# Optimization experiments

Measured on AMD Instinct MI355X. Metric: run time of the kernel, lower is better.

## Reference

```python
import jax, jax.numpy as jnp
import numpy as np

BS, NC, CN, DN = 8, 1024, 64, 64
GH, GW = 32, 32
ALPHA, BPC = 4, 4
G = 8
IN_LO, IN_HI = 0, ALPHA
OUT_LO, OUT_HI = ALPHA, 2 * ALPHA
B_LO, B_HI = 2 * ALPHA, 2 * ALPHA + BPC
HS, HM, HMOD = 256, 256, 128
MOD_IN = 3 * DN + 2 + BPC
MOD_OUT = DN + BPC


def setup_inputs():
    key = jax.random.key(0)
    ks = iter(jax.random.split(key, 40))
    def nrm(shape, s=0.05):
        return jax.random.normal(next(ks), shape, dtype=jnp.float32) * s
    return {
        "x": nrm((BS, NC * DN), 1.0),
        "h": nrm((BS, NC, CN, DN), 0.01),
        "msg": nrm((BS, NC, CN, DN), 0.1),
        "W": nrm((BS, NC, CN, CN), 0.1),
        "decay_logit": jnp.zeros((BS, NC, CN), jnp.float32),
        "cell_context": jnp.zeros((BS, NC, DN), jnp.float32),
        "border_gate_logit": jnp.zeros((BS, NC, BPC), jnp.float32),
        "neuron_id": nrm((NC, CN, DN), 0.02),
        "state_w1": nrm((HS, 2 * DN)), "state_b1": jnp.zeros((HS,), jnp.float32),
        "state_gs1": jnp.ones((G, HS), jnp.float32), "state_gb1": jnp.zeros((G, HS), jnp.float32),
        "state_w2": nrm((DN, HS)), "state_b2": jnp.zeros((DN,), jnp.float32),
        "state_gs2": jnp.ones((G, DN), jnp.float32), "state_gb2": jnp.zeros((G, DN), jnp.float32),
        "msg_w1": nrm((HM, DN)), "msg_b1": jnp.zeros((HM,), jnp.float32),
        "msg_gs1": jnp.ones((G, HM), jnp.float32), "msg_gb1": jnp.zeros((G, HM), jnp.float32),
        "msg_w2": nrm((DN, HM)), "msg_b2": jnp.zeros((DN,), jnp.float32),
        "msg_gs2": jnp.ones((G, DN), jnp.float32), "msg_gb2": jnp.zeros((G, DN), jnp.float32),
        "inject_w": nrm((G, ALPHA * DN, DN)), "inject_b": jnp.zeros((G, ALPHA * DN), jnp.float32),
        "mod_w1": nrm((NC, MOD_IN, HMOD)), "mod_b1": jnp.zeros((NC, HMOD), jnp.float32),
        "mod_w2": nrm((NC, HMOD, MOD_OUT), 0.01), "mod_b2": jnp.zeros((NC, MOD_OUT), jnp.float32),
        "cell_to_group": jnp.arange(NC, dtype=jnp.int32) % G,
    }


def _grouped_mlp(x, c2g, w1, b1, gs1, gb1, w2, b2, gs2, gb2):
    # x: [B, NC, CN, F]; group-specific affine modulation after each linear.
    hid = jnp.einsum('bcnf,hf->bcnh', x, w1) + b1
    hid = jnp.tanh(hid * gs1[c2g][None, :, None, :] + gb1[c2g][None, :, None, :])
    out = jnp.einsum('bcnh,dh->bcnd', hid, w2) + b2
    return jnp.tanh(out * gs2[c2g][None, :, None, :] + gb2[c2g][None, :, None, :])


def reference(x, h, msg, W, decay_logit, cell_context, border_gate_logit, neuron_id,
              state_w1, state_b1, state_gs1, state_gb1, state_w2, state_b2, state_gs2, state_gb2,
              msg_w1, msg_b1, msg_gs1, msg_gb1, msg_w2, msg_b2, msg_gs2, msg_gb2,
              inject_w, inject_b, mod_w1, mod_b1, mod_w2, mod_b2, cell_to_group):
    c2g = cell_to_group
    # 1) dense message passing inside each cell: received = W @ msg
    received = jnp.einsum('bcnm,bcmd->bcnd', W, msg)
    # 2) inject external input into input ports (per-group orthogonal-init projections)
    cell_slice = x.reshape(BS, NC, DN)
    iw, ib = inject_w[c2g], inject_b[c2g]                      # [NC, alpha*DN, DN], [NC, alpha*DN]
    inject = jnp.einsum('bni,noi->bno', cell_slice, iw) + ib   # [BS, NC, alpha*DN]
    received = received.at[:, :, IN_LO:IN_HI].add(inject.reshape(BS, NC, ALPHA, DN))
    # 3) fixed geometric border exchange between neighboring grid cells
    border = msg[:, :, B_LO:B_HI].reshape(BS, GH, GW, BPC, DN)
    incoming = jnp.zeros_like(border)
    incoming = incoming.at[:, 1:, :, 0].set(border[:, :-1, :, 1])
    incoming = incoming.at[:, :-1, :, 1].set(border[:, 1:, :, 0])
    incoming = incoming.at[:, :, 1:, 2].set(border[:, :, :-1, 3])
    incoming = incoming.at[:, :, :-1, 3].set(border[:, :, 1:, 2])
    incoming = incoming.reshape(BS, NC, BPC, DN)
    border_gate = jax.nn.sigmoid(border_gate_logit)[..., None]
    received = received.at[:, :, B_LO:B_HI].add(border_gate * incoming)
    # 4) gated recurrent state update
    decay = jax.nn.sigmoid(decay_logit)[..., None]
    cand = _grouped_mlp(jnp.concatenate([received, h], axis=-1), c2g,
                        state_w1, state_b1, state_gs1, state_gb1,
                        state_w2, state_b2, state_gs2, state_gb2)
    h_new = decay * h + (1.0 - decay) * cand
    # 5) emit new messages (+ per-neuron identity embedding)
    msg_new = _grouped_mlp(h_new, c2g, msg_w1, msg_b1, msg_gs1, msg_gb1,
                           msg_w2, msg_b2, msg_gs2, msg_gb2) + neuron_id[None]
    # 6) readout from output ports
    readout = (msg_new[:, :, OUT_LO:OUT_HI].sum(axis=2) * (ALPHA ** -0.5)).reshape(BS, -1)
    # 7) per-cell modulation MLP (distinct weights per cell)
    h_mean = h_new.mean(axis=2)
    msg_mean = msg_new.mean(axis=2)
    W_row = jnp.abs(W).mean(axis=-1).mean(axis=2, keepdims=True)
    decay_mean = decay_logit.mean(axis=2, keepdims=True)
    feats = jnp.concatenate([h_mean, msg_mean, W_row, decay_mean,
                             cell_context, border_gate_logit], axis=-1)   # [BS, NC, MOD_IN]
    hid = jnp.tanh(jnp.einsum('bcf,cfh->bch', feats, mod_w1) + mod_b1)
    mod = jnp.einsum('bch,cho->bco', hid, mod_w2) + mod_b2                 # [BS, NC, MOD_OUT]
    cell_context_new = cell_context + mod[..., :DN]
    border_gate_logit_new = border_gate_logit + mod[..., DN:]
    return readout, h_new, msg_new, cell_context_new, border_gate_logit_new
```

## Files before the change

kernel.cpp:

```cpp
#include <hip/hip_runtime.h>

#define NCC 1024
#define MODIN 198
#define MODOUT 68
#define HMODL 128

typedef __attribute__((ext_vector_type(8))) short s8v;
typedef __attribute__((ext_vector_type(4))) float f4v;
typedef unsigned short ushort_t;
typedef unsigned int uint_t;

#define OFF_SW1 0
#define OFF_SW2 32768
#define OFF_MW1 49152
#define OFF_MW2 65536
#define FEATS_BYTE_OFF 262144

__device__ __forceinline__ float fast_tanh(float x) {
    const float e = __builtin_amdgcn_exp2f(x * 2.885390081777927f);
    const float r = __builtin_amdgcn_rcpf(e + 1.f);
    return fmaf(-2.f, r, 1.f);
}
__device__ __forceinline__ float fast_sigmoid(float x) {
    const float e = __builtin_amdgcn_exp2f(x * -1.4426950408889634f);
    return __builtin_amdgcn_rcpf(e + 1.f);
}
__device__ __forceinline__ ushort_t f2bf(float x) {
    uint_t u = __builtin_bit_cast(uint_t, x);
    u += 0x7FFFu + ((u >> 16) & 1u);
    return (ushort_t)(u >> 16);
}
__device__ __forceinline__ uint_t pk2(float a, float b) {
    return (uint_t)f2bf(a) | ((uint_t)f2bf(b) << 16);
}
#define SWZ(byteoff, row) ((byteoff) ^ (((row) & 7) << 4))

__global__ __launch_bounds__(256)
void mg_cvtw(const float* __restrict__ sw1, const float* __restrict__ sw2,
             const float* __restrict__ mw1, const float* __restrict__ mw2,
             ushort_t* __restrict__ o) {
    const int i = blockIdx.x * 256 + threadIdx.x;
    float v;
    if (i < 32768)      v = sw1[i];
    else if (i < 49152) v = sw2[i - 32768];
    else if (i < 65536) v = mw1[i - 49152];
    else                v = mw2[i - 65536];
    o[i] = f2bf(v);
}

__global__ __launch_bounds__(256, 4)
void mg_inject(const float* __restrict__ xp, const float* __restrict__ iw,
               const float* __restrict__ ibias, const int* __restrict__ c2g,
               float* __restrict__ injb) {
    const int c = blockIdx.x, t = threadIdx.x;
    const int g = c2g[c];
    __shared__ float s_x[8][64];
    for (int idx = t; idx < 512; idx += 256)
        s_x[idx >> 6][idx & 63] = xp[(size_t)(idx >> 6) * (NCC * 64) + c * 64 + (idx & 63)];
    __syncthreads();
    const float* wrow = iw + (size_t)g * 16384 + t * 64;
    float a0 = 0.f, a1 = 0.f, a2 = 0.f, a3 = 0.f, a4 = 0.f, a5 = 0.f, a6 = 0.f, a7 = 0.f;
    #pragma unroll
    for (int i = 0; i < 64; i += 4) {
        const float4 w4 = *(const float4*)(wrow + i);
        const float4 x0 = *(const float4*)&s_x[0][i];
        const float4 x1 = *(const float4*)&s_x[1][i];
        const float4 x2 = *(const float4*)&s_x[2][i];
        const float4 x3 = *(const float4*)&s_x[3][i];
        const float4 x4 = *(const float4*)&s_x[4][i];
        const float4 x5 = *(const float4*)&s_x[5][i];
        const float4 x6 = *(const float4*)&s_x[6][i];
        const float4 x7 = *(const float4*)&s_x[7][i];
        a0 = fmaf(w4.x, x0.x, a0); a0 = fmaf(w4.y, x0.y, a0); a0 = fmaf(w4.z, x0.z, a0); a0 = fmaf(w4.w, x0.w, a0);
        a1 = fmaf(w4.x, x1.x, a1); a1 = fmaf(w4.y, x1.y, a1); a1 = fmaf(w4.z, x1.z, a1); a1 = fmaf(w4.w, x1.w, a1);
        a2 = fmaf(w4.x, x2.x, a2); a2 = fmaf(w4.y, x2.y, a2); a2 = fmaf(w4.z, x2.z, a2); a2 = fmaf(w4.w, x2.w, a2);
        a3 = fmaf(w4.x, x3.x, a3); a3 = fmaf(w4.y, x3.y, a3); a3 = fmaf(w4.z, x3.z, a3); a3 = fmaf(w4.w, x3.w, a3);
        a4 = fmaf(w4.x, x4.x, a4); a4 = fmaf(w4.y, x4.y, a4); a4 = fmaf(w4.z, x4.z, a4); a4 = fmaf(w4.w, x4.w, a4);
        a5 = fmaf(w4.x, x5.x, a5); a5 = fmaf(w4.y, x5.y, a5); a5 = fmaf(w4.z, x5.z, a5); a5 = fmaf(w4.w, x5.w, a5);
        a6 = fmaf(w4.x, x6.x, a6); a6 = fmaf(w4.y, x6.y, a6); a6 = fmaf(w4.z, x6.z, a6); a6 = fmaf(w4.w, x6.w, a6);
        a7 = fmaf(w4.x, x7.x, a7); a7 = fmaf(w4.y, x7.y, a7); a7 = fmaf(w4.z, x7.z, a7); a7 = fmaf(w4.w, x7.w, a7);
    }
    const float bv = ibias[g * 256 + t];
    const float acc[8] = {a0, a1, a2, a3, a4, a5, a6, a7};
    #pragma unroll
    for (int b = 0; b < 8; b++)
        injb[((size_t)b * NCC + c) * 4096 + t] = acc[b] + bv;
}

__global__ __launch_bounds__(512, 4)
void mg_cell_kernel(
    const float* __restrict__ hp,   const float* __restrict__ msgp,
    const float* __restrict__ Wp,   const float* __restrict__ decayp,
    const float* __restrict__ bglp, const float* __restrict__ nidp,
    const float* __restrict__ sb1,  const float* __restrict__ sgs1,
    const float* __restrict__ sgb1, const float* __restrict__ sb2,
    const float* __restrict__ sgs2, const float* __restrict__ sgb2,
    const float* __restrict__ mb1,  const float* __restrict__ mgs1,
    const float* __restrict__ mgb1, const float* __restrict__ mb2,
    const float* __restrict__ mgs2, const float* __restrict__ mgb2,
    const int*   __restrict__ c2g,  const ushort_t* __restrict__ wb,
    float* __restrict__ out_read, float* __restrict__ out_h,
    float* __restrict__ out_msg,  float* __restrict__ wsf)
{
    const int t  = threadIdx.x;
    const int bc = blockIdx.x;
    const int b  = bc >> 10, c = bc & 1023;
    const int gh = c >> 5, gwc = c & 31;
    const int lane = t & 63, w = t >> 6;
    const int cl = lane & 15, q = lane >> 4;
    const int g  = c2g[c];
    const size_t tile = (size_t)bc * 4096;

    __shared__ ushort_t sHid[8192];
    __shared__ ushort_t sIn[8192];
    __shared__ float s_scr[256];
    __shared__ float s_dec[64];
    __shared__ float s_wsum[8];
    __shared__ float s_dsum;

    ushort_t* sW    = sHid;
    ushort_t* sMsgT = sHid + 4096;

    {
        const int n = t >> 3, m0 = (t & 7) * 8;
        const float* src = Wp + tile + n * 64 + m0;
        const float4 v0 = *(const float4*)(src);
        const float4 v1 = *(const float4*)(src + 4);
        float wsum = fabsf(v0.x) + fabsf(v0.y) + fabsf(v0.z) + fabsf(v0.w)
                   + fabsf(v1.x) + fabsf(v1.y) + fabsf(v1.z) + fabsf(v1.w);
        *(uint_t*)((char*)sW + SWZ(n * 128 + (m0 + 0) * 2, n)) = pk2(v0.x, v0.y);
        *(uint_t*)((char*)sW + SWZ(n * 128 + (m0 + 2) * 2, n)) = pk2(v0.z, v0.w);
        *(uint_t*)((char*)sW + SWZ(n * 128 + (m0 + 4) * 2, n)) = pk2(v1.x, v1.y);
        *(uint_t*)((char*)sW + SWZ(n * 128 + (m0 + 6) * 2, n)) = pk2(v1.z, v1.w);
        #pragma unroll
        for (int off = 32; off > 0; off >>= 1) wsum += __shfl_down(wsum, off);
        if (lane == 0) s_wsum[w] = wsum;
    }
    #pragma unroll
    for (int i = 0; i < 2; i++) {
        const int m = (t >> 4) + i * 32, d0 = (t & 15) * 4;
        const float4 v = *(const float4*)(msgp + tile + (size_t)m * 64 + d0);
        *(ushort_t*)((char*)sMsgT + SWZ((d0 + 0) * 128 + m * 2, d0 + 0)) = f2bf(v.x);
        *(ushort_t*)((char*)sMsgT + SWZ((d0 + 1) * 128 + m * 2, d0 + 1)) = f2bf(v.y);
        *(ushort_t*)((char*)sMsgT + SWZ((d0 + 2) * 128 + m * 2, d0 + 2)) = f2bf(v.z);
        *(ushort_t*)((char*)sMsgT + SWZ((d0 + 3) * 128 + m * 2, d0 + 3)) = f2bf(v.w);
    }
    #pragma unroll
    for (int i = 0; i < 2; i++) {
        const int n = (t >> 4) + i * 32, d0 = (t & 15) * 4;
        const float4 v = *(const float4*)(hp + tile + (size_t)n * 64 + d0);
        *(uint_t*)((char*)sIn + SWZ(n * 256 + (64 + d0) * 2, n))     = pk2(v.x, v.y);
        *(uint_t*)((char*)sIn + SWZ(n * 256 + (64 + d0 + 2) * 2, n)) = pk2(v.z, v.w);
    }
    if (t < 256) {
        const int p = w, dd = lane;
        int ok, nc2, qq;
        if      (p == 0) { ok = (gh > 0);   nc2 = c - 32; qq = 1; }
        else if (p == 1) { ok = (gh < 31);  nc2 = c + 32; qq = 0; }
        else if (p == 2) { ok = (gwc > 0);  nc2 = c - 1;  qq = 3; }
        else             { ok = (gwc < 31); nc2 = c + 1;  qq = 2; }
        float v = 0.f;
        if (ok) v = msgp[((size_t)b * NCC + nc2) * 4096 + (8 + qq) * 64 + dd];
        s_scr[p * 64 + dd] = fast_sigmoid(bglp[(size_t)bc * 4 + p]) * v;
    }
    if (w == 4) {
        const float dl = decayp[(size_t)bc * 64 + lane];
        s_dec[lane] = fast_sigmoid(dl);
        float v = dl;
        #pragma unroll
        for (int off = 32; off > 0; off >>= 1) v += __shfl_down(v, off);
        if (lane == 0) s_dsum = v;
    }
    __syncthreads();

    const f4v fzero = {0.f, 0.f, 0.f, 0.f};
    const int d  = 16 * (w & 3) + cl;
    const int rh = w >> 2;

    {
        f4v wm[2] = {fzero, fzero};
        float injv[4] = {0.f, 0.f, 0.f, 0.f};
        if (rh == 0 && q == 0) {
            #pragma unroll
            for (int r = 0; r < 4; r++) injv[r] = out_h[tile + r * 64 + d];
        }
        __builtin_amdgcn_s_setprio(1);
        #pragma unroll
        for (int ks = 0; ks < 2; ks++) {
            const int k0 = ks * 32 + q * 8;
            const s8v bf = *(const s8v*)((const char*)sMsgT + SWZ(d * 128 + k0 * 2, d));
            #pragma unroll
            for (int rt2 = 0; rt2 < 2; rt2++) {
                const int ar = (rh * 2 + rt2) * 16 + cl;
                const s8v af = *(const s8v*)((const char*)sW + SWZ(ar * 128 + k0 * 2, ar));
                wm[rt2] = __builtin_amdgcn_mfma_f32_16x16x32_bf16(af, bf, wm[rt2], 0, 0, 0);
            }
        }
        __builtin_amdgcn_s_setprio(0);
        #pragma unroll
        for (int rt2 = 0; rt2 < 2; rt2++)
            #pragma unroll
            for (int r = 0; r < 4; r++) {
                const int n = (rh * 2 + rt2) * 16 + q * 4 + r;
                float v = wm[rt2][r];
                if (n < 4)                 v += injv[r];
                else if (n >= 8 && n < 12) v += s_scr[(n - 8) * 64 + d];
                *(ushort_t*)((char*)sIn + SWZ(n * 256 + d * 2, n)) = f2bf(v);
            }
    }
    __syncthreads();

    {
        f4v a2[2][2];
        a2[0][0] = fzero; a2[0][1] = fzero; a2[1][0] = fzero; a2[1][1] = fzero;
        const ushort_t* wb1 = wb + OFF_SW1;
        const ushort_t* wb2 = wb + OFF_SW2;
        #pragma unroll
        for (int p = 0; p < 2; p++) {
            {
                f4v acc[4] = {fzero, fzero, fzero, fzero};
                const int lc = 16 * w + cl;
                const int hcol = p * 128 + lc;
                __builtin_amdgcn_s_setprio(1);
                #pragma unroll
                for (int ks = 0; ks < 4; ks++) {
                    const int k0 = ks * 32 + q * 8;
                    const s8v bf = *(const s8v*)(wb1 + (size_t)hcol * 128 + k0);
                    #pragma unroll
                    for (int rt = 0; rt < 4; rt++) {
                        const int ar = rt * 16 + cl;
                        const s8v af = *(const s8v*)((const char*)sIn + SWZ(ar * 256 + k0 * 2, ar));
                        acc[rt] = __builtin_amdgcn_mfma_f32_16x16x32_bf16(af, bf, acc[rt], 0, 0, 0);
                    }
                }
                __builtin_amdgcn_s_setprio(0);
                const float b1 = sb1[hcol], g1 = sgs1[g * 256 + hcol], o1 = sgb1[g * 256 + hcol];
                #pragma unroll
                for (int rt = 0; rt < 4; rt++)
                    #pragma unroll
                    for (int r = 0; r < 4; r++) {
                        const int n = rt * 16 + q * 4 + r;
                        const float vv = fast_tanh(fmaf(acc[rt][r] + b1, g1, o1));
                        *(ushort_t*)((char*)sHid + SWZ(n * 256 + lc * 2, n)) = f2bf(vv);
                    }
            }
            __syncthreads();
            {
                __builtin_amdgcn_s_setprio(1);
                #pragma unroll
                for (int ks = 0; ks < 4; ks++) {
                    const int k0 = ks * 32 + q * 8;
                    const s8v bf = *(const s8v*)(wb2 + (size_t)d * 256 + p * 128 + k0);
                    #pragma unroll
                    for (int rt2 = 0; rt2 < 2; rt2++) {
                        const int ar = (rh * 2 + rt2) * 16 + cl;
                        const s8v af = *(const s8v*)((const char*)sHid + SWZ(ar * 256 + k0 * 2, ar));
                        a2[rt2][ks & 1] = __builtin_amdgcn_mfma_f32_16x16x32_bf16(af, bf, a2[rt2][ks & 1], 0, 0, 0);
                    }
                }
                __builtin_amdgcn_s_setprio(0);
            }
            if (p == 0) __syncthreads();
        }
        const float b2 = sb2[d], g2 = sgs2[g * 64 + d], o2 = sgb2[g * 64 + d];
        float hsum = 0.f;
        #pragma unroll
        for (int rt2 = 0; rt2 < 2; rt2++)
            #pragma unroll
            for (int r = 0; r < 4; r++) {
                const int n = (rh * 2 + rt2) * 16 + q * 4 + r;
                const float cand = fast_tanh(fmaf(a2[rt2][0][r] + a2[rt2][1][r] + b2, g2, o2));
                const ushort_t hu = *(const ushort_t*)((const char*)sIn + SWZ(n * 256 + (64 + d) * 2, n));
                const float hv = __builtin_bit_cast(float, (uint_t)hu << 16);
                const float hn = fmaf(s_dec[n], hv - cand, cand);
                out_h[tile + (size_t)n * 64 + d] = hn;
                *(ushort_t*)((char*)sIn + SWZ(n * 256 + d * 2, n)) = f2bf(hn);
                hsum += hn;
            }
        hsum += __shfl_xor(hsum, 16);
        hsum += __shfl_xor(hsum, 32);
        if (q == 0) s_scr[rh * 64 + d] = hsum;
    }
    __syncthreads();

    {
        float nv[8];
        #pragma unroll
        for (int rt2 = 0; rt2 < 2; rt2++)
            #pragma unroll
            for (int r = 0; r < 4; r++) {
                const int n = (rh * 2 + rt2) * 16 + q * 4 + r;
                nv[rt2 * 4 + r] = nidp[(size_t)c * 4096 + (size_t)n * 64 + d];
            }
        f4v a6[2][2];
        a6[0][0] = fzero; a6[0][1] = fzero; a6[1][0] = fzero; a6[1][1] = fzero;
        const ushort_t* wm1 = wb + OFF_MW1;
        const ushort_t* wm2 = wb + OFF_MW2;
        #pragma unroll
        for (int p = 0; p < 2; p++) {
            {
                f4v acc[4] = {fzero, fzero, fzero, fzero};
                const int lc = 16 * w + cl;
                const int hcol = p * 128 + lc;
                __builtin_amdgcn_s_setprio(1);
                #pragma unroll
                for (int ks = 0; ks < 2; ks++) {
                    const int k0 = ks * 32 + q * 8;
                    const s8v bf = *(const s8v*)(wm1 + (size_t)hcol * 64 + k0);
                    #pragma unroll
                    for (int rt = 0; rt < 4; rt++) {
                        const int ar = rt * 16 + cl;
                        const s8v af = *(const s8v*)((const char*)sIn + SWZ(ar * 256 + k0 * 2, ar));
                        acc[rt] = __builtin_amdgcn_mfma_f32_16x16x32_bf16(af, bf, acc[rt], 0, 0, 0);
                    }
                }
                __builtin_amdgcn_s_setprio(0);
                const float b1 = mb1[hcol], g1 = mgs1[g * 256 + hcol], o1 = mgb1[g * 256 + hcol];
                #pragma unroll
                for (int rt = 0; rt < 4; rt++)
                    #pragma unroll
                    for (int r = 0; r < 4; r++) {
                        const int n = rt * 16 + q * 4 + r;
                        const float vv = fast_tanh(fmaf(acc[rt][r] + b1, g1, o1));
                        *(ushort_t*)((char*)sHid + SWZ(n * 256 + lc * 2, n)) = f2bf(vv);
                    }
            }
            __syncthreads();
            {
                __builtin_amdgcn_s_setprio(1);
                #pragma unroll
                for (int ks = 0; ks < 4; ks++) {
                    const int k0 = ks * 32 + q * 8;
                    const s8v bf = *(const s8v*)(wm2 + (size_t)d * 256 + p * 128 + k0);
                    #pragma unroll
                    for (int rt2 = 0; rt2 < 2; rt2++) {
                        const int ar = (rh * 2 + rt2) * 16 + cl;
                        const s8v af = *(const s8v*)((const char*)sHid + SWZ(ar * 256 + k0 * 2, ar));
                        a6[rt2][ks & 1] = __builtin_amdgcn_mfma_f32_16x16x32_bf16(af, bf, a6[rt2][ks & 1], 0, 0, 0);
                    }
                }
                __builtin_amdgcn_s_setprio(0);
            }
            if (p == 0) __syncthreads();
        }
        const float b2 = mb2[d], g2 = mgs2[g * 64 + d], o2 = mgb2[g * 64 + d];
        float msum = 0.f, ro = 0.f;
        #pragma unroll
        for (int rt2 = 0; rt2 < 2; rt2++)
            #pragma unroll
            for (int r = 0; r < 4; r++) {
                const int n = (rh * 2 + rt2) * 16 + q * 4 + r;
                const float mv = fast_tanh(fmaf(a6[rt2][0][r] + a6[rt2][1][r] + b2, g2, o2))
                                 + nv[rt2 * 4 + r];
                out_msg[tile + (size_t)n * 64 + d] = mv;
                msum += mv;
                if (rt2 == 0 && q == 1 && rh == 0) ro += mv;
            }
        msum += __shfl_xor(msum, 16);
        msum += __shfl_xor(msum, 32);
        if (q == 0) s_scr[128 + rh * 64 + d] = msum;
        if (rh == 0 && q == 1) out_read[((size_t)b * NCC + c) * 64 + d] = ro * 0.5f;
    }
    __syncthreads();

    if (t < 132) {
        float v = 0.f;
        if (t < 64)        v = (s_scr[t] + s_scr[64 + t]) * (1.f / 64.f);
        else if (t < 128)  v = (s_scr[64 + t] + s_scr[128 + t]) * (1.f / 64.f);
        else if (t == 128) v = (s_wsum[0] + s_wsum[1] + s_wsum[2] + s_wsum[3]
                              + s_wsum[4] + s_wsum[5] + s_wsum[6] + s_wsum[7]) * (1.f / 4096.f);
        else if (t == 129) v = s_dsum * (1.f / 64.f);
        wsf[(size_t)bc * 132 + t] = v;
    }
}

__global__ __launch_bounds__(256, 2)
void mg_mod_kernel(
    const float* __restrict__ wsf,   const float* __restrict__ modw1,
    const float* __restrict__ modb1, const float* __restrict__ modw2,
    const float* __restrict__ modb2, const float* __restrict__ ctxp,
    const float* __restrict__ bglp,  float* __restrict__ out_ctx,
    float* __restrict__ out_bg)
{
    const int c = blockIdx.x;
    const int t = threadIdx.x;
    __shared__ float s_f[8][MODIN];
    __shared__ float s_h2[8][HMODL];

    for (int k = t; k < 8 * MODIN; k += 256) {
        const int b = k / MODIN, f = k - b * MODIN;
        float v;
        if (f < 130)      v = wsf[((size_t)b * NCC + c) * 132 + f];
        else if (f < 194) v = ctxp[((size_t)b * NCC + c) * 64 + (f - 130)];
        else              v = bglp[((size_t)b * NCC + c) * 4 + (f - 194)];
        s_f[b][f] = v;
    }
    __syncthreads();

    {
        const int hh = t & 127, bh = (t >> 7) * 4;
        float a0 = 0.f, a1 = 0.f, a2 = 0.f, a3 = 0.f;
        const float* wp = modw1 + (size_t)c * MODIN * HMODL + hh;
        for (int f = 0; f < MODIN; f++) {
            const float wv = wp[(size_t)f * HMODL];
            a0 = fmaf(s_f[bh + 0][f], wv, a0);
            a1 = fmaf(s_f[bh + 1][f], wv, a1);
            a2 = fmaf(s_f[bh + 2][f], wv, a2);
            a3 = fmaf(s_f[bh + 3][f], wv, a3);
        }
        const float bv = modb1[(size_t)c * HMODL + hh];
        s_h2[bh + 0][hh] = fast_tanh(a0 + bv);
        s_h2[bh + 1][hh] = fast_tanh(a1 + bv);
        s_h2[bh + 2][hh] = fast_tanh(a2 + bv);
        s_h2[bh + 3][hh] = fast_tanh(a3 + bv);
    }
    __syncthreads();

    for (int idx = t; idx < 8 * MODOUT; idx += 256) {
        const int b = idx / MODOUT, o = idx - b * MODOUT;
        float acc = modb2[(size_t)c * MODOUT + o];
        const float* wp = modw2 + (size_t)c * HMODL * MODOUT + o;
        const float* hrow = s_h2[b];
        for (int hh = 0; hh < HMODL; hh++)
            acc = fmaf(hrow[hh], wp[(size_t)hh * MODOUT], acc);
        if (o < 64)
            out_ctx[((size_t)b * NCC + c) * 64 + o] =
                ctxp[((size_t)b * NCC + c) * 64 + o] + acc;
        else
            out_bg[((size_t)b * NCC + c) * 4 + (o - 64)] =
                bglp[((size_t)b * NCC + c) * 4 + (o - 64)] + acc;
    }
}

extern "C" void kernel_launch(void* const* d_in, const int* in_sizes, int n_in,
                              void* d_out, int out_size, void* d_ws, size_t ws_size,
                              hipStream_t stream) {
    const float* xp     = (const float*)d_in[0];
    const float* hp     = (const float*)d_in[1];
    const float* msgp   = (const float*)d_in[2];
    const float* Wp     = (const float*)d_in[3];
    const float* decayp = (const float*)d_in[4];
    const float* ctxp   = (const float*)d_in[5];
    const float* bglp   = (const float*)d_in[6];
    const float* nidp   = (const float*)d_in[7];
    const float* sw1    = (const float*)d_in[8];
    const float* sb1    = (const float*)d_in[9];
    const float* sgs1   = (const float*)d_in[10];
    const float* sgb1   = (const float*)d_in[11];
    const float* sw2    = (const float*)d_in[12];
    const float* sb2    = (const float*)d_in[13];
    const float* sgs2   = (const float*)d_in[14];
    const float* sgb2   = (const float*)d_in[15];
    const float* mw1    = (const float*)d_in[16];
    const float* mb1    = (const float*)d_in[17];
    const float* mgs1   = (const float*)d_in[18];
    const float* mgb1   = (const float*)d_in[19];
    const float* mw2    = (const float*)d_in[20];
    const float* mb2    = (const float*)d_in[21];
    const float* mgs2   = (const float*)d_in[22];
    const float* mgb2   = (const float*)d_in[23];
    const float* iw     = (const float*)d_in[24];
    const float* ibias  = (const float*)d_in[25];
    const float* modw1  = (const float*)d_in[26];
    const float* modb1  = (const float*)d_in[27];
    const float* modw2  = (const float*)d_in[28];
    const float* modb2  = (const float*)d_in[29];
    const int*   c2g    = (const int*)d_in[30];

    float* out      = (float*)d_out;
    float* out_read = out;
    float* out_h    = out_read + 524288;
    float* out_msg  = out_h + 33554432;
    float* out_ctx  = out_msg + 33554432;
    float* out_bg   = out_ctx + 524288;

    ushort_t* wb  = (ushort_t*)d_ws;
    float*    wsf = (float*)((char*)d_ws + FEATS_BYTE_OFF);

    mg_cvtw<<<320, 256, 0, stream>>>(sw1, sw2, mw1, mw2, wb);

    mg_inject<<<1024, 256, 0, stream>>>(xp, iw, ibias, c2g, out_h);

    mg_cell_kernel<<<8192, 512, 0, stream>>>(
        hp, msgp, Wp, decayp, bglp, nidp,
        sb1, sgs1, sgb1, sb2, sgs2, sgb2,
        mb1, mgs1, mgb1, mb2, mgs2, mgb2,
        c2g, wb, out_read, out_h, out_msg, wsf);

    mg_mod_kernel<<<1024, 256, 0, stream>>>(
        wsf, modw1, modb1, modw2, modb2, ctxp, bglp, out_ctx, out_bg);
}
```

Measured before the change: 465.5 us.

## Swap MFMA operand roles so accumulators hold contiguous features for vectorized stores

Transposes every MFMA in the step kernel by swapping the A and B operands, so each lane's four accumulator values span four consecutive feature columns instead of four neuron rows. This lets the epilogues use float4 global loads and stores for h, msg, neuron_id and readout, packed 64-bit bf16 LDS writes, and float4 bias/scale loads. It replaces scattered scalar stores and 2-byte LDS writes with wider accesses. In exchange, the row reductions need a 4-step 16-lane shuffle tree per component instead of two shuffles, plus extra shuffles for the readout sum.

```diff
diff --git a/kernel.cpp b/kernel.cpp
--- a/kernel.cpp
+++ b/kernel.cpp
@@ -174,39 +174,39 @@
     __syncthreads();
 
     const f4v fzero = {0.f, 0.f, 0.f, 0.f};
-    const int d  = 16 * (w & 3) + cl;
+    const int d0 = 16 * (w & 3) + q * 4;
+    const int dA = 16 * (w & 3) + cl;
     const int rh = w >> 2;
 
     {
         f4v wm[2] = {fzero, fzero};
-        float injv[4] = {0.f, 0.f, 0.f, 0.f};
-        if (rh == 0 && q == 0) {
-            #pragma unroll
-            for (int r = 0; r < 4; r++) injv[r] = out_h[tile + r * 64 + d];
-        }
         __builtin_amdgcn_s_setprio(1);
         #pragma unroll
         for (int ks = 0; ks < 2; ks++) {
             const int k0 = ks * 32 + q * 8;
-            const s8v bf = *(const s8v*)((const char*)sMsgT + SWZ(d * 128 + k0 * 2, d));
+            const s8v am = *(const s8v*)((const char*)sMsgT + SWZ(dA * 128 + k0 * 2, dA));
             #pragma unroll
-            for (int rt2 = 0; rt2 < 2; rt2++) {
-                const int ar = (rh * 2 + rt2) * 16 + cl;
-                const s8v af = *(const s8v*)((const char*)sW + SWZ(ar * 128 + k0 * 2, ar));
-                wm[rt2] = __builtin_amdgcn_mfma_f32_16x16x32_bf16(af, bf, wm[rt2], 0, 0, 0);
+            for (int nt = 0; nt < 2; nt++) {
+                const int ar = (rh * 2 + nt) * 16 + cl;
+                const s8v bw = *(const s8v*)((const char*)sW + SWZ(ar * 128 + k0 * 2, ar));
+                wm[nt] = __builtin_amdgcn_mfma_f32_16x16x32_bf16(am, bw, wm[nt], 0, 0, 0);
             }
         }
         __builtin_amdgcn_s_setprio(0);
         #pragma unroll
-        for (int rt2 = 0; rt2 < 2; rt2++)
-            #pragma unroll
-            for (int r = 0; r < 4; r++) {
-                const int n = (rh * 2 + rt2) * 16 + q * 4 + r;
-                float v = wm[rt2][r];
-                if (n < 4)                 v += injv[r];
-                else if (n >= 8 && n < 12) v += s_scr[(n - 8) * 64 + d];
-                *(ushort_t*)((char*)sIn + SWZ(n * 256 + d * 2, n)) = f2bf(v);
-            }
+        for (int nt = 0; nt < 2; nt++) {
+            const int n = (rh * 2 + nt) * 16 + cl;
+            float v0 = wm[nt][0], v1 = wm[nt][1], v2 = wm[nt][2], v3 = wm[nt][3];
+            if (n < 4) {
+                const float4 inj = *(const float4*)(out_h + tile + (size_t)n * 64 + d0);
+                v0 += inj.x; v1 += inj.y; v2 += inj.z; v3 += inj.w;
+            } else if (n >= 8 && n < 12) {
+                const float4 bin = *(const float4*)&s_scr[(n - 8) * 64 + d0];
+                v0 += bin.x; v1 += bin.y; v2 += bin.z; v3 += bin.w;
+            }
+            uint2 pkd; pkd.x = pk2(v0, v1); pkd.y = pk2(v2, v3);
+            *(uint2*)((char*)sIn + SWZ(n * 256 + d0 * 2, n)) = pkd;
+        }
     }
     __syncthreads();
 
@@ -219,30 +219,35 @@
         for (int p = 0; p < 2; p++) {
             {
                 f4v acc[4] = {fzero, fzero, fzero, fzero};
-                const int lc = 16 * w + cl;
-                const int hcol = p * 128 + lc;
+                const int hrow = p * 128 + 16 * w + cl;
                 __builtin_amdgcn_s_setprio(1);
                 #pragma unroll
                 for (int ks = 0; ks < 4; ks++) {
                     const int k0 = ks * 32 + q * 8;
-                    const s8v bf = *(const s8v*)(wb1 + (size_t)hcol * 128 + k0);
+                    const s8v aw = *(const s8v*)(wb1 + (size_t)hrow * 128 + k0);
                     #pragma unroll
                     for (int rt = 0; rt < 4; rt++) {
                         const int ar = rt * 16 + cl;
-                        const s8v af = *(const s8v*)((const char*)sIn + SWZ(ar * 256 + k0 * 2, ar));
-                        acc[rt] = __builtin_amdgcn_mfma_f32_16x16x32_bf16(af, bf, acc[rt], 0, 0, 0);
+                        const s8v bi = *(const s8v*)((const char*)sIn + SWZ(ar * 256 + k0 * 2, ar));
+                        acc[rt] = __builtin_amdgcn_mfma_f32_16x16x32_bf16(aw, bi, acc[rt], 0, 0, 0);
                     }
                 }
                 __builtin_amdgcn_s_setprio(0);
-                const float b1 = sb1[hcol], g1 = sgs1[g * 256 + hcol], o1 = sgb1[g * 256 + hcol];
+                const int hc0 = p * 128 + 16 * w + q * 4;
+                const float4 b1 = *(const float4*)&sb1[hc0];
+                const float4 g1 = *(const float4*)&sgs1[g * 256 + hc0];
+                const float4 o1 = *(const float4*)&sgb1[g * 256 + hc0];
+                const int lc0 = 16 * w + q * 4;
                 #pragma unroll
-                for (int rt = 0; rt < 4; rt++)
-                    #pragma unroll
-                    for (int r = 0; r < 4; r++) {
-                        const int n = rt * 16 + q * 4 + r;
-                        const float vv = fast_tanh(fmaf(acc[rt][r] + b1, g1, o1));
-                        *(ushort_t*)((char*)sHid + SWZ(n * 256 + lc * 2, n)) = f2bf(vv);
-                    }
+                for (int rt = 0; rt < 4; rt++) {
+                    const int n = rt * 16 + cl;
+                    const float t0 = fast_tanh(fmaf(acc[rt][0] + b1.x, g1.x, o1.x));
+                    const float t1 = fast_tanh(fmaf(acc[rt][1] + b1.y, g1.y, o1.y));
+                    const float t2 = fast_tanh(fmaf(acc[rt][2] + b1.z, g1.z, o1.z));
+                    const float t3 = fast_tanh(fmaf(acc[rt][3] + b1.w, g1.w, o1.w));
+                    uint2 pkd; pkd.x = pk2(t0, t1); pkd.y = pk2(t2, t3);
+                    *(uint2*)((char*)sHid + SWZ(n * 256 + lc0 * 2, n)) = pkd;
+                }
             }
             __syncthreads();
             {
@@ -250,48 +255,58 @@
                 #pragma unroll
                 for (int ks = 0; ks < 4; ks++) {
                     const int k0 = ks * 32 + q * 8;
-                    const s8v bf = *(const s8v*)(wb2 + (size_t)d * 256 + p * 128 + k0);
+                    const s8v aw = *(const s8v*)(wb2 + (size_t)dA * 256 + p * 128 + k0);
                     #pragma unroll
-                    for (int rt2 = 0; rt2 < 2; rt2++) {
-                        const int ar = (rh * 2 + rt2) * 16 + cl;
-                        const s8v af = *(const s8v*)((const char*)sHid + SWZ(ar * 256 + k0 * 2, ar));
-                        a2[rt2][ks & 1] = __builtin_amdgcn_mfma_f32_16x16x32_bf16(af, bf, a2[rt2][ks & 1], 0, 0, 0);
+                    for (int nt = 0; nt < 2; nt++) {
+                        const int ar = (rh * 2 + nt) * 16 + cl;
+                        const s8v bh = *(const s8v*)((const char*)sHid + SWZ(ar * 256 + k0 * 2, ar));
+                        a2[nt][ks & 1] = __builtin_amdgcn_mfma_f32_16x16x32_bf16(aw, bh, a2[nt][ks & 1], 0, 0, 0);
                     }
                 }
                 __builtin_amdgcn_s_setprio(0);
             }
             if (p == 0) __syncthreads();
         }
-        const float b2 = sb2[d], g2 = sgs2[g * 64 + d], o2 = sgb2[g * 64 + d];
-        float hsum = 0.f;
-        #pragma unroll
-        for (int rt2 = 0; rt2 < 2; rt2++)
-            #pragma unroll
-            for (int r = 0; r < 4; r++) {
-                const int n = (rh * 2 + rt2) * 16 + q * 4 + r;
-                const float cand = fast_tanh(fmaf(a2[rt2][0][r] + a2[rt2][1][r] + b2, g2, o2));
-                const ushort_t hu = *(const ushort_t*)((const char*)sIn + SWZ(n * 256 + (64 + d) * 2, n));
-                const float hv = __builtin_bit_cast(float, (uint_t)hu << 16);
-                const float hn = fmaf(s_dec[n], hv - cand, cand);
-                out_h[tile + (size_t)n * 64 + d] = hn;
-                *(ushort_t*)((char*)sIn + SWZ(n * 256 + d * 2, n)) = f2bf(hn);
-                hsum += hn;
-            }
-        hsum += __shfl_xor(hsum, 16);
-        hsum += __shfl_xor(hsum, 32);
-        if (q == 0) s_scr[rh * 64 + d] = hsum;
+        const float4 b2 = *(const float4*)&sb2[d0];
+        const float4 g2 = *(const float4*)&sgs2[g * 64 + d0];
+        const float4 o2 = *(const float4*)&sgb2[g * 64 + d0];
+        float hs0 = 0.f, hs1 = 0.f, hs2 = 0.f, hs3 = 0.f;
+        #pragma unroll
+        for (int nt = 0; nt < 2; nt++) {
+            const int n = (rh * 2 + nt) * 16 + cl;
+            const float dec = s_dec[n];
+            const uint2 hu = *(const uint2*)((const char*)sIn + SWZ(n * 256 + (64 + d0) * 2, n));
+            const float hv0 = __builtin_bit_cast(float, (uint_t)(hu.x << 16));
+            const float hv1 = __builtin_bit_cast(float, hu.x & 0xFFFF0000u);
+            const float hv2 = __builtin_bit_cast(float, (uint_t)(hu.y << 16));
+            const float hv3 = __builtin_bit_cast(float, hu.y & 0xFFFF0000u);
+            const float c0 = fast_tanh(fmaf(a2[nt][0][0] + a2[nt][1][0] + b2.x, g2.x, o2.x));
+            const float c1 = fast_tanh(fmaf(a2[nt][0][1] + a2[nt][1][1] + b2.y, g2.y, o2.y));
+            const float c2 = fast_tanh(fmaf(a2[nt][0][2] + a2[nt][1][2] + b2.z, g2.z, o2.z));
+            const float c3 = fast_tanh(fmaf(a2[nt][0][3] + a2[nt][1][3] + b2.w, g2.w, o2.w));
+            float4 hn;
+            hn.x = fmaf(dec, hv0 - c0, c0);
+            hn.y = fmaf(dec, hv1 - c1, c1);
+            hn.z = fmaf(dec, hv2 - c2, c2);
+            hn.w = fmaf(dec, hv3 - c3, c3);
+            *(float4*)(out_h + tile + (size_t)n * 64 + d0) = hn;
+            uint2 pkd; pkd.x = pk2(hn.x, hn.y); pkd.y = pk2(hn.z, hn.w);
+            *(uint2*)((char*)sIn + SWZ(n * 256 + d0 * 2, n)) = pkd;
+            hs0 += hn.x; hs1 += hn.y; hs2 += hn.z; hs3 += hn.w;
+        }
+        #pragma unroll
+        for (int m = 1; m < 16; m <<= 1) {
+            hs0 += __shfl_xor(hs0, m); hs1 += __shfl_xor(hs1, m);
+            hs2 += __shfl_xor(hs2, m); hs3 += __shfl_xor(hs3, m);
+        }
+        if (cl == 0) {
+            float4 hp4 = {hs0, hs1, hs2, hs3};
+            *(float4*)&s_scr[rh * 64 + d0] = hp4;
+        }
     }
     __syncthreads();
 
     {
-        float nv[8];
-        #pragma unroll
-        for (int rt2 = 0; rt2 < 2; rt2++)
-            #pragma unroll
-            for (int r = 0; r < 4; r++) {
-                const int n = (rh * 2 + rt2) * 16 + q * 4 + r;
-                nv[rt2 * 4 + r] = nidp[(size_t)c * 4096 + (size_t)n * 64 + d];
-            }
         f4v a6[2][2];
         a6[0][0] = fzero; a6[0][1] = fzero; a6[1][0] = fzero; a6[1][1] = fzero;
         const ushort_t* wm1 = wb + OFF_MW1;
@@ -300,30 +315,35 @@
         for (int p = 0; p < 2; p++) {
             {
                 f4v acc[4] = {fzero, fzero, fzero, fzero};
-                const int lc = 16 * w + cl;
-                const int hcol = p * 128 + lc;
+                const int hrow = p * 128 + 16 * w + cl;
                 __builtin_amdgcn_s_setprio(1);
                 #pragma unroll
                 for (int ks = 0; ks < 2; ks++) {
                     const int k0 = ks * 32 + q * 8;
-                    const s8v bf = *(const s8v*)(wm1 + (size_t)hcol * 64 + k0);
+                    const s8v aw = *(const s8v*)(wm1 + (size_t)hrow * 64 + k0);
                     #pragma unroll
                     for (int rt = 0; rt < 4; rt++) {
                         const int ar = rt * 16 + cl;
-                        const s8v af = *(const s8v*)((const char*)sIn + SWZ(ar * 256 + k0 * 2, ar));
-                        acc[rt] = __builtin_amdgcn_mfma_f32_16x16x32_bf16(af, bf, acc[rt], 0, 0, 0);
+                        const s8v bi = *(const s8v*)((const char*)sIn + SWZ(ar * 256 + k0 * 2, ar));
+                        acc[rt] = __builtin_amdgcn_mfma_f32_16x16x32_bf16(aw, bi, acc[rt], 0, 0, 0);
                     }
                 }
                 __builtin_amdgcn_s_setprio(0);
-                const float b1 = mb1[hcol], g1 = mgs1[g * 256 + hcol], o1 = mgb1[g * 256 + hcol];
+                const int hc0 = p * 128 + 16 * w + q * 4;
+                const float4 b1 = *(const float4*)&mb1[hc0];
+                const float4 g1 = *(const float4*)&mgs1[g * 256 + hc0];
+                const float4 o1 = *(const float4*)&mgb1[g * 256 + hc0];
+                const int lc0 = 16 * w + q * 4;
                 #pragma unroll
-                for (int rt = 0; rt < 4; rt++)
-                    #pragma unroll
-                    for (int r = 0; r < 4; r++) {
-                        const int n = rt * 16 + q * 4 + r;
-                        const float vv = fast_tanh(fmaf(acc[rt][r] + b1, g1, o1));
-                        *(ushort_t*)((char*)sHid + SWZ(n * 256 + lc * 2, n)) = f2bf(vv);
-                    }
+                for (int rt = 0; rt < 4; rt++) {
+                    const int n = rt * 16 + cl;
+                    const float t0 = fast_tanh(fmaf(acc[rt][0] + b1.x, g1.x, o1.x));
+                    const float t1 = fast_tanh(fmaf(acc[rt][1] + b1.y, g1.y, o1.y));
+                    const float t2 = fast_tanh(fmaf(acc[rt][2] + b1.z, g1.z, o1.z));
+                    const float t3 = fast_tanh(fmaf(acc[rt][3] + b1.w, g1.w, o1.w));
+                    uint2 pkd; pkd.x = pk2(t0, t1); pkd.y = pk2(t2, t3);
+                    *(uint2*)((char*)sHid + SWZ(n * 256 + lc0 * 2, n)) = pkd;
+                }
             }
             __syncthreads();
             {
@@ -331,35 +351,55 @@
                 #pragma unroll
                 for (int ks = 0; ks < 4; ks++) {
                     const int k0 = ks * 32 + q * 8;
-                    const s8v bf = *(const s8v*)(wm2 + (size_t)d * 256 + p * 128 + k0);
+                    const s8v aw = *(const s8v*)(wm2 + (size_t)dA * 256 + p * 128 + k0);
                     #pragma unroll
-                    for (int rt2 = 0; rt2 < 2; rt2++) {
-                        const int ar = (rh * 2 + rt2) * 16 + cl;
-                        const s8v af = *(const s8v*)((const char*)sHid + SWZ(ar * 256 + k0 * 2, ar));
-                        a6[rt2][ks & 1] = __builtin_amdgcn_mfma_f32_16x16x32_bf16(af, bf, a6[rt2][ks & 1], 0, 0, 0);
+                    for (int nt = 0; nt < 2; nt++) {
+                        const int ar = (rh * 2 + nt) * 16 + cl;
+                        const s8v bh = *(const s8v*)((const char*)sHid + SWZ(ar * 256 + k0 * 2, ar));
+                        a6[nt][ks & 1] = __builtin_amdgcn_mfma_f32_16x16x32_bf16(aw, bh, a6[nt][ks & 1], 0, 0, 0);
                     }
                 }
                 __builtin_amdgcn_s_setprio(0);
             }
             if (p == 0) __syncthreads();
         }
-        const float b2 = mb2[d], g2 = mgs2[g * 64 + d], o2 = mgb2[g * 64 + d];
-        float msum = 0.f, ro = 0.f;
-        #pragma unroll
-        for (int rt2 = 0; rt2 < 2; rt2++)
-            #pragma unroll
-            for (int r = 0; r < 4; r++) {
-                const int n = (rh * 2 + rt2) * 16 + q * 4 + r;
-                const float mv = fast_tanh(fmaf(a6[rt2][0][r] + a6[rt2][1][r] + b2, g2, o2))
-                                 + nv[rt2 * 4 + r];
-                out_msg[tile + (size_t)n * 64 + d] = mv;
-                msum += mv;
-                if (rt2 == 0 && q == 1 && rh == 0) ro += mv;
-            }
-        msum += __shfl_xor(msum, 16);
-        msum += __shfl_xor(msum, 32);
-        if (q == 0) s_scr[128 + rh * 64 + d] = msum;
-        if (rh == 0 && q == 1) out_read[((size_t)b * NCC + c) * 64 + d] = ro * 0.5f;
+        const float4 b2 = *(const float4*)&mb2[d0];
+        const float4 g2 = *(const float4*)&mgs2[g * 64 + d0];
+        const float4 o2 = *(const float4*)&mgb2[g * 64 + d0];
+        float ms0 = 0.f, ms1 = 0.f, ms2 = 0.f, ms3 = 0.f;
+        float ro0 = 0.f, ro1 = 0.f, ro2 = 0.f, ro3 = 0.f;
+        #pragma unroll
+        for (int nt = 0; nt < 2; nt++) {
+            const int n = (rh * 2 + nt) * 16 + cl;
+            const float4 nv = *(const float4*)(nidp + (size_t)c * 4096 + (size_t)n * 64 + d0);
+            float4 mv;
+            mv.x = fast_tanh(fmaf(a6[nt][0][0] + a6[nt][1][0] + b2.x, g2.x, o2.x)) + nv.x;
+            mv.y = fast_tanh(fmaf(a6[nt][0][1] + a6[nt][1][1] + b2.y, g2.y, o2.y)) + nv.y;
+            mv.z = fast_tanh(fmaf(a6[nt][0][2] + a6[nt][1][2] + b2.z, g2.z, o2.z)) + nv.z;
+            mv.w = fast_tanh(fmaf(a6[nt][0][3] + a6[nt][1][3] + b2.w, g2.w, o2.w)) + nv.w;
+            *(float4*)(out_msg + tile + (size_t)n * 64 + d0) = mv;
+            ms0 += mv.x; ms1 += mv.y; ms2 += mv.z; ms3 += mv.w;
+            if (nt == 0 && rh == 0 && n >= 4 && n < 8) {
+                ro0 = mv.x; ro1 = mv.y; ro2 = mv.z; ro3 = mv.w;
+            }
+        }
+        #pragma unroll
+        for (int m = 1; m < 16; m <<= 1) {
+            ms0 += __shfl_xor(ms0, m); ms1 += __shfl_xor(ms1, m);
+            ms2 += __shfl_xor(ms2, m); ms3 += __shfl_xor(ms3, m);
+        }
+        if (cl == 0) {
+            float4 mp4 = {ms0, ms1, ms2, ms3};
+            *(float4*)&s_scr[128 + rh * 64 + d0] = mp4;
+        }
+        ro0 += __shfl_xor(ro0, 1); ro1 += __shfl_xor(ro1, 1);
+        ro2 += __shfl_xor(ro2, 1); ro3 += __shfl_xor(ro3, 1);
+        ro0 += __shfl_xor(ro0, 2); ro1 += __shfl_xor(ro1, 2);
+        ro2 += __shfl_xor(ro2, 2); ro3 += __shfl_xor(ro3, 2);
+        if (rh == 0 && cl == 4) {
+            float4 o4 = {ro0 * 0.5f, ro1 * 0.5f, ro2 * 0.5f, ro3 * 0.5f};
+            *(float4*)(out_read + ((size_t)b * NCC + c) * 64 + d0) = o4;
+        }
     }
     __syncthreads();
 
```

Result: faster. 446.0 us (-4.2%).
